# Kernel tuning notes

Measured on AMD Instinct MI355X. Metric: run time of the kernel, lower is better.

Reference implementation:

```python
import jax, jax.numpy as jnp
import numpy as np

B, L, D = 128, 512, 768   # batch, bert tokens, bert hidden
J = 32                    # clause boundaries -> S = J + 1 segments
S = J + 1
DM, DF = 200, 200         # transformer d_model / ffn dim
EPS = 1e-5


def _ln(x, g, b):
    m = x.mean(-1, keepdims=True)
    v = ((x - m) ** 2).mean(-1, keepdims=True)
    return (x - m) / jnp.sqrt(v + EPS) * g + b


def setup_inputs() -> dict:
    key = jax.random.key(0)
    ks = jax.random.split(key, 12)
    sc = 0.02
    hidden_state = jax.random.normal(ks[0], (B, L, D), jnp.float32)
    # strictly increasing, positive clause boundaries < L (non-empty segments)
    seg = L // S  # stride ~= 15 tokens per clause
    jitter = jax.random.randint(ks[1], (B, J), 0, seg).astype(jnp.int32)
    clause_idx = jnp.arange(1, J + 1, dtype=jnp.int32)[None, :] * seg + jitter
    p = lambda k, shp: sc * jax.random.normal(k, shp, jnp.float32)
    z = lambda n: jnp.zeros((n,), jnp.float32)
    return {
        'hidden_state': hidden_state,
        'clause_idx': clause_idx,
        'fc5_w': p(ks[2], (1, D)), 'fc5_b': z(1),
        'fc1_w': p(ks[3], (DM, D)), 'fc1_b': z(DM),
        'attn_in_w': p(ks[4], (3 * DM, DM)), 'attn_in_b': z(3 * DM),
        'attn_out_w': p(ks[5], (DM, DM)), 'attn_out_b': z(DM),
        'ln1_g': jnp.ones((DM,), jnp.float32), 'ln1_b': z(DM),
        'lin1_w': p(ks[6], (DF, DM)), 'lin1_b': z(DF),
        'lin2_w': p(ks[7], (DM, DF)), 'lin2_b': z(DM),
        'ln2_g': jnp.ones((DM,), jnp.float32), 'ln2_b': z(DM),
        'fc_w': p(ks[8], (2, 2 * DM)), 'fc_b': z(2),
    }


def reference(hidden_state, clause_idx, fc5_w, fc5_b, fc1_w, fc1_b,
              attn_in_w, attn_in_b, attn_out_w, attn_out_b,
              ln1_g, ln1_b, lin1_w, lin1_b, lin2_w, lin2_b,
              ln2_g, ln2_b, fc_w, fc_b):
    # ---- ragged per-segment attention pooling (batched_index_select) ----
    t = jnp.arange(L)
    # segment id of each token: number of boundaries <= t  -> [B, L] in [0, S)
    seg_id = jnp.sum(t[None, None, :] >= clause_idx[:, :, None], axis=1)
    scores = jnp.einsum('bld,d->bl', hidden_state, fc5_w[0]) + fc5_b[0]  # fc5
    mask = seg_id[:, None, :] == jnp.arange(S)[None, :, None]            # [B,S,L]
    logits = jnp.where(mask, scores[:, None, :], -jnp.inf)
    w = jax.nn.softmax(logits, axis=-1)        # per-segment softmax over tokens
    pooled = jnp.einsum('bsl,bld->bsd', w, hidden_state)                 # [B,S,D]

    # ---- fc1 + TransformerEncoderLayer (post-norm, 1 head, relu, no dropout)
    x = pooled @ fc1_w.T + fc1_b                                         # [B,S,DM]
    qkv = x @ attn_in_w.T + attn_in_b
    q, k, v = jnp.split(qkv, 3, axis=-1)
    a = jax.nn.softmax(jnp.einsum('bqd,bkd->bqk', q, k) * (1.0 / np.sqrt(DM).item()), axis=-1)
    att = jnp.einsum('bqk,bkd->bqd', a, v) @ attn_out_w.T + attn_out_b
    x = _ln(x + att, ln1_g, ln1_b)
    ff = jax.nn.relu(x @ lin1_w.T + lin1_b) @ lin2_w.T + lin2_b
    x = _ln(x + ff, ln2_g, ln2_b)

    # ---- cat(first-token broadcast, rest) then classifier fc ----
    h = jnp.concatenate([jnp.broadcast_to(x[:, :1, :], (B, S - 1, DM)), x[:, 1:, :]], axis=-1)
    return h @ fc_w.T + fc_b                                             # [B, S-1, 2]
```

## Files before the change

### kernel.cpp

```cpp
#include <hip/hip_runtime.h>

#define NB 128
#define LL 512
#define DD 768
#define JJ 32
#define SS 33
#define DM 200

typedef __attribute__((ext_vector_type(8))) short bf8_t;
typedef __attribute__((ext_vector_type(4))) float f4_t;

#define SB_XF   0
#define SB_QB   61440
#define SB_KB   82944
#define SB_VT   104448
#define SB_Y2   235520
#define SB_BLK  275456

static __device__ __forceinline__ unsigned short f2bf(float f) {
  unsigned u = __float_as_uint(f);
  return (unsigned short)((u + 0x7FFFu + ((u >> 16) & 1u)) >> 16);
}

template<int KS>
static __device__ __forceinline__ f4_t mfma_tile(
    const unsigned short* pa, const unsigned short* pw)
{
  f4_t acc = {0.f, 0.f, 0.f, 0.f};
  bf8_t a = *(const bf8_t*)pa;
  bf8_t w = *(const bf8_t*)pw;
#pragma unroll
  for (int s = 1; s < KS; ++s) {
    bf8_t a2 = *(const bf8_t*)(pa + 32 * s);
    bf8_t w2 = *(const bf8_t*)(pw + 32 * s);
    acc = __builtin_amdgcn_mfma_f32_16x16x32_bf16(a, w, acc, 0, 0, 0);
    a = a2; w = w2;
  }
  acc = __builtin_amdgcn_mfma_f32_16x16x32_bf16(a, w, acc, 0, 0, 0);
  return acc;
}

template<int KS>
static __device__ __forceinline__ f4_t mfma_tile_lds(
    const unsigned short* pa, const unsigned short* pw)
{
  f4_t acc = {0.f, 0.f, 0.f, 0.f};
#pragma unroll
  for (int s = 0; s < KS; ++s) {
    bf8_t a = *(const bf8_t*)(pa + 32 * s);
    bf8_t w = *(const bf8_t*)(pw + 32 * s);
    acc = __builtin_amdgcn_mfma_f32_16x16x32_bf16(a, w, acc, 0, 0, 0);
  }
  return acc;
}

__global__ __launch_bounds__(512) void pc_kernel(
    const float* __restrict__ hidden, const int* __restrict__ clause,
    const float* __restrict__ fc5w, unsigned short* __restrict__ pooled_bf,
    const float* __restrict__ fc1_w, const float* __restrict__ ain_w,
    const float* __restrict__ aout_w, const float* __restrict__ lin1_w,
    const float* __restrict__ lin2_w,
    unsigned short* __restrict__ fc1_wb, unsigned short* __restrict__ ain_wb,
    unsigned short* __restrict__ aout_wb, unsigned short* __restrict__ lin1_wb,
    unsigned short* __restrict__ lin2_wb, char* __restrict__ scratch)
{
  const int tid = threadIdx.x;
  if (blockIdx.x >= NB * SS) {
    int t = (blockIdx.x - NB * SS) * 512 + tid;
    if (t < 208 * 768) {
      int n = t / 768, k = t - n * 768;
      fc1_wb[t] = f2bf((n < 200) ? fc1_w[n * 768 + k] : 0.f);
      return;
    }
    t -= 208 * 768;
    if (t < 608 * 224) {
      int n = t / 224, k = t - n * 224;
      ain_wb[t] = f2bf((n < 600 && k < 200) ? ain_w[n * 200 + k] : 0.f);
      return;
    }
    t -= 608 * 224;
    if (t < 208 * 224) {
      int n = t / 224, k = t - n * 224;
      aout_wb[t] = f2bf((n < 200 && k < 200) ? aout_w[n * 200 + k] : 0.f);
      return;
    }
    t -= 208 * 224;
    if (t < 208 * 224) {
      int n = t / 224, k = t - n * 224;
      lin1_wb[t] = f2bf((n < 200 && k < 200) ? lin1_w[n * 200 + k] : 0.f);
      return;
    }
    t -= 208 * 224;
    if (t < 208 * 224) {
      int n = t / 224, k = t - n * 224;
      lin2_wb[t] = f2bf((n < 200 && k < 200) ? lin2_w[n * 200 + k] : 0.f);
      return;
    }
    t -= 208 * 224;
    if (t < NB * 1344) {
      int b = t / 1344, r = t - b * 1344;
      char* sb = scratch + (size_t)b * SB_BLK;
      const uint4 z = make_uint4(0, 0, 0, 0);
      if (r < 384) {
        int bi = r / 192, rr = r - bi * 192;
        int row = rr >> 2, c = rr & 3;
        int off = (bi == 0) ? SB_QB : SB_KB;
        *(uint4*)((unsigned short*)(sb + off) + row * 224 + 192 + c * 8) = z;
      } else {
        int rr = r - 384;
        int row = rr >> 2, c = rr & 3;
        *(uint4*)((unsigned short*)(sb + SB_VT) + row * 64 + 32 + c * 8) = z;
      }
    }
    return;
  }

  int blk = blockIdx.x;
  int b = blk / SS;
  int s = blk - b * SS;
  int t0 = (s == 0) ? 0 : clause[b * JJ + s - 1];
  int t1 = (s == JJ) ? LL : clause[b * JJ + s];
  int nt = t1 - t0;
  if (nt > 64) nt = 64;
  if (nt < 1) nt = 1;

  __shared__ float wsm[64];
  int wave = tid >> 6, lane = tid & 63;

  const float4* w4 = (const float4*)fc5w;
  for (int t = t0 + wave; t < t0 + nt; t += 8) {
    const float4* hp = (const float4*)(hidden + ((long long)b * LL + t) * DD);
    float acc = 0.f;
#pragma unroll
    for (int i = 0; i < 3; ++i) {
      float4 h = hp[lane + 64 * i];
      float4 w = w4[lane + 64 * i];
      acc += h.x * w.x + h.y * w.y + h.z * w.z + h.w * w.w;
    }
#pragma unroll
    for (int off = 32; off; off >>= 1) acc += __shfl_xor(acc, off);
    if (lane == 0) wsm[t - t0] = acc;
  }
  __syncthreads();

  if (wave == 0) {
    float v = (lane < nt) ? wsm[lane] : -__builtin_inff();
    float mx = v;
#pragma unroll
    for (int off = 32; off; off >>= 1) mx = fmaxf(mx, __shfl_xor(mx, off));
    float e = (lane < nt) ? __expf(v - mx) : 0.f;
    float sm = e;
#pragma unroll
    for (int off = 32; off; off >>= 1) sm += __shfl_xor(sm, off);
    if (lane < nt) wsm[lane] = e / sm;
  }
  __syncthreads();

  if (tid < 384) {
    const float2* base = (const float2*)(hidden + ((long long)b * LL + t0) * DD);
    float2 acc = make_float2(0.f, 0.f);
#pragma unroll 4
    for (int t = 0; t < nt; ++t) {
      float w = wsm[t];
      float2 h = base[t * 384 + tid];
      acc.x = fmaf(w, h.x, acc.x);
      acc.y = fmaf(w, h.y, acc.y);
    }
    ushort2 o;
    o.x = f2bf(acc.x); o.y = f2bf(acc.y);
    *(ushort2*)(pooled_bf + (long long)blk * DD + tid * 2) = o;
  }
}

__global__ __launch_bounds__(512) void k_fc1qkv(
    const unsigned short* __restrict__ pooled,
    const unsigned short* __restrict__ fc1_wb, const float* __restrict__ fc1_b,
    const unsigned short* __restrict__ ain_wb, const float* __restrict__ ain_b,
    char* __restrict__ scratch)
{
  const int b = blockIdx.x / 3, mt = blockIdx.x % 3, m0 = mt * 16;
  const int tid = threadIdx.x, wv = tid >> 6, lane = tid & 63;
  const int col = lane & 15, quad = lane >> 4, koff = quad * 8;

  char* sb = scratch + (size_t)b * SB_BLK;
  float* x_f32 = (float*)(sb + SB_XF);
  unsigned short* q_bf  = (unsigned short*)(sb + SB_QB);
  unsigned short* k_bf  = (unsigned short*)(sb + SB_KB);
  unsigned short* vt_bf = (unsigned short*)(sb + SB_VT);

  __shared__ __align__(16) unsigned short xb[16][232];
  for (int u = tid; u < 16 * 16; u += 512) {
    int row = u >> 4, c = u & 15;
    ((unsigned*)&xb[row][200])[c] = 0u;
  }

  const unsigned short* Ab = pooled + (size_t)b * SS * DD;
  for (int t = wv; t < 13; t += 8) {
    int n0 = t * 16;
    f4_t acc = mfma_tile<24>(Ab + (size_t)(m0 + col) * DD + koff,
                             fc1_wb + (size_t)(n0 + col) * DD + koff);
    int gn = n0 + col;
    if (gn < DM) {
      float bv = fc1_b[gn];
#pragma unroll
      for (int r = 0; r < 4; ++r) {
        int row = quad * 4 + r;
        float v = acc[r] + bv;
        x_f32[(m0 + row) * 208 + gn] = v;
        xb[row][gn] = f2bf(v);
      }
    }
  }
  __syncthreads();

  for (int t = wv; t < 38; t += 8) {
    int n0 = t * 16;
    f4_t acc = mfma_tile_lds<7>(&xb[0][0] + col * 232 + koff,
                                ain_wb + (size_t)(n0 + col) * 224 + koff);
    int gn = n0 + col;
    if (gn < 600) {
      float bv = ain_b[gn];
#pragma unroll
      for (int r = 0; r < 4; ++r) {
        int gm = m0 + quad * 4 + r;
        unsigned short bfv = f2bf(acc[r] + bv);
        if (gn < 200)      q_bf[gm * 224 + gn] = bfv;
        else if (gn < 400) k_bf[gm * 224 + (gn - 200)] = bfv;
        else if (gm < SS)  vt_bf[(gn - 400) * 64 + gm] = bfv;
      }
    }
  }
}

__global__ __launch_bounds__(512) void k_postattn(
    const unsigned short* __restrict__ aout_wb, const float* __restrict__ aout_b,
    const float* __restrict__ ln1_g, const float* __restrict__ ln1_b,
    const unsigned short* __restrict__ lin1_wb, const float* __restrict__ lin1_b,
    const unsigned short* __restrict__ lin2_wb, const float* __restrict__ lin2_b,
    const float* __restrict__ ln2_g, const float* __restrict__ ln2_b,
    char* __restrict__ scratch)
{
  const int b = blockIdx.x / 3, mt = blockIdx.x % 3, m0 = mt * 16;
  const int tid = threadIdx.x, wv = tid >> 6, lane = tid & 63;
  const int col = lane & 15, quad = lane >> 4, koff = quad * 8;

  char* sb = scratch + (size_t)b * SB_BLK;
  const unsigned short* q_bf  = (const unsigned short*)(sb + SB_QB);
  const unsigned short* k_bf  = (const unsigned short*)(sb + SB_KB);
  const unsigned short* vt_bf = (const unsigned short*)(sb + SB_VT);
  const float* x_f32 = (const float*)(sb + SB_XF);
  float* y2g = (float*)(sb + SB_Y2);

  __shared__ float tc[16][211];
  __shared__ __align__(16) unsigned short Pb[16][72];
  __shared__ __align__(16) unsigned short yb[16][232];
  __shared__ __align__(16) unsigned short fb[16][232];
  for (int u = tid; u < 16 * 16; u += 512) {
    int row = u >> 4, c = u & 15;
    ((unsigned*)&yb[row][200])[c] = 0u;
    ((unsigned*)&fb[row][200])[c] = 0u;
  }

  for (int t = wv; t < 3; t += 8) {
    int n0 = t * 16;
    f4_t acc = mfma_tile<7>(q_bf + (m0 + col) * 224 + koff,
                            k_bf + (n0 + col) * 224 + koff);
    int gn = n0 + col;
#pragma unroll
    for (int r = 0; r < 4; ++r)
      tc[quad * 4 + r][gn] = acc[r] * 0.07071067811865475f;
  }
  __syncthreads();

  for (int r = wv; r < 16; r += 8) {
    bool live = (m0 + r) < SS;
    float v = (lane < SS && live) ? tc[r][lane] : -__builtin_inff();
    float mx = v;
#pragma unroll
    for (int off = 32; off; off >>= 1) mx = fmaxf(mx, __shfl_xor(mx, off));
    float e = (lane < SS && live) ? __expf(v - mx) : 0.f;
    float sm = e;
#pragma unroll
    for (int off = 32; off; off >>= 1) sm += __shfl_xor(sm, off);
    Pb[r][lane] = (lane < SS && live) ? f2bf(e / sm) : (unsigned short)0;
  }
  __syncthreads();

  for (int t = wv; t < 13; t += 8) {
    int n0 = t * 16;
    f4_t acc = mfma_tile_lds<2>(&Pb[0][0] + col * 72 + koff,
                                vt_bf + (n0 + col) * 64 + koff);
    int gn = n0 + col;
    if (gn < DM) {
#pragma unroll
      for (int r = 0; r < 4; ++r)
        fb[quad * 4 + r][gn] = f2bf(acc[r]);
    }
  }
  __syncthreads();

  for (int t = wv; t < 13; t += 8) {
    int n0 = t * 16;
    f4_t acc = mfma_tile_lds<7>(&fb[0][0] + col * 232 + koff,
                                aout_wb + (size_t)(n0 + col) * 224 + koff);
    int gn = n0 + col;
    float bv = (gn < DM) ? aout_b[gn] : 0.f;
#pragma unroll
    for (int r = 0; r < 4; ++r) {
      int row = quad * 4 + r;
      float v = acc[r] + bv;
      if (gn < DM) v += x_f32[(m0 + row) * 208 + gn];
      tc[row][gn] = v;
    }
  }
  __syncthreads();

  for (int r = wv; r < 16; r += 8) {
    float* p = &tc[r][0];
    float vals[4]; float s = 0.f;
#pragma unroll
    for (int i = 0; i < 4; ++i) { int k = lane + 64 * i; vals[i] = (k < DM) ? p[k] : 0.f; s += vals[i]; }
#pragma unroll
    for (int off = 32; off; off >>= 1) s += __shfl_xor(s, off);
    float mean = s * (1.f / DM);
    float vs = 0.f;
#pragma unroll
    for (int i = 0; i < 4; ++i) { int k = lane + 64 * i; if (k < DM) { float d = vals[i] - mean; vs += d * d; } }
#pragma unroll
    for (int off = 32; off; off >>= 1) vs += __shfl_xor(vs, off);
    float rstd = rsqrtf(vs * (1.f / DM) + 1e-5f);
#pragma unroll
    for (int i = 0; i < 4; ++i) {
      int k = lane + 64 * i;
      if (k < DM) {
        float o = (vals[i] - mean) * rstd * ln1_g[k] + ln1_b[k];
        p[k] = o;
        yb[r][k] = f2bf(o);
      }
    }
  }
  __syncthreads();

  for (int t = wv; t < 13; t += 8) {
    int n0 = t * 16;
    f4_t acc = mfma_tile_lds<7>(&yb[0][0] + col * 232 + koff,
                                lin1_wb + (size_t)(n0 + col) * 224 + koff);
    int gn = n0 + col;
    if (gn < DM) {
      float bv = lin1_b[gn];
#pragma unroll
      for (int r = 0; r < 4; ++r)
        fb[quad * 4 + r][gn] = f2bf(fmaxf(acc[r] + bv, 0.f));
    }
  }
  __syncthreads();

  for (int t = wv; t < 13; t += 8) {
    int n0 = t * 16;
    f4_t acc = mfma_tile_lds<7>(&fb[0][0] + col * 232 + koff,
                                lin2_wb + (size_t)(n0 + col) * 224 + koff);
    int gn = n0 + col;
    if (gn < DM) {
      float bv = lin2_b[gn];
#pragma unroll
      for (int r = 0; r < 4; ++r) {
        int row = quad * 4 + r;
        tc[row][gn] = acc[r] + bv + tc[row][gn];
      }
    }
  }
  __syncthreads();

  for (int r = wv; r < 16; r += 8) {
    float* p = &tc[r][0];
    float vals[4]; float s = 0.f;
#pragma unroll
    for (int i = 0; i < 4; ++i) { int k = lane + 64 * i; vals[i] = (k < DM) ? p[k] : 0.f; s += vals[i]; }
#pragma unroll
    for (int off = 32; off; off >>= 1) s += __shfl_xor(s, off);
    float mean = s * (1.f / DM);
    float vs = 0.f;
#pragma unroll
    for (int i = 0; i < 4; ++i) { int k = lane + 64 * i; if (k < DM) { float d = vals[i] - mean; vs += d * d; } }
#pragma unroll
    for (int off = 32; off; off >>= 1) vs += __shfl_xor(vs, off);
    float rstd = rsqrtf(vs * (1.f / DM) + 1e-5f);
    int grow = m0 + r;
#pragma unroll
    for (int i = 0; i < 4; ++i) {
      int k = lane + 64 * i;
      if (k < DM) y2g[grow * 208 + k] = (vals[i] - mean) * rstd * ln2_g[k] + ln2_b[k];
    }
  }
}

__global__ __launch_bounds__(256) void k_cls(
    const char* __restrict__ scratch, const float* __restrict__ fcw,
    const float* __restrict__ fcb, float* __restrict__ out)
{
  int gw = blockIdx.x * 4 + (threadIdx.x >> 6);
  int lane = threadIdx.x & 63;
  int b = gw >> 5, j = gw & 31;
  const float* y2 = (const float*)(scratch + (size_t)b * SB_BLK + SB_Y2);
  const float* r0 = y2;
  const float* rj = y2 + (1 + j) * 208;
  float a0 = 0.f, a1 = 0.f;
  for (int k = lane; k < DM; k += 64) {
    float u = r0[k], w = rj[k];
    a0 += u * fcw[k]       + w * fcw[200 + k];
    a1 += u * fcw[400 + k] + w * fcw[600 + k];
  }
#pragma unroll
  for (int off = 32; off; off >>= 1) {
    a0 += __shfl_xor(a0, off);
    a1 += __shfl_xor(a1, off);
  }
  if (lane == 0) {
    out[gw * 2 + 0] = a0 + fcb[0];
    out[gw * 2 + 1] = a1 + fcb[1];
  }
}

extern "C" void kernel_launch(void* const* d_in, const int* in_sizes, int n_in,
                              void* d_out, int out_size, void* d_ws, size_t ws_size,
                              hipStream_t stream)
{
  (void)in_sizes; (void)n_in; (void)out_size; (void)ws_size;
  const float* hidden = (const float*)d_in[0];
  const int*   clause = (const int*)d_in[1];
  const float* fc5_w  = (const float*)d_in[2];
  const float* fc1_w  = (const float*)d_in[4];
  const float* fc1_b  = (const float*)d_in[5];
  const float* ain_w  = (const float*)d_in[6];
  const float* ain_b  = (const float*)d_in[7];
  const float* aout_w = (const float*)d_in[8];
  const float* aout_b = (const float*)d_in[9];
  const float* ln1_g  = (const float*)d_in[10];
  const float* ln1_b  = (const float*)d_in[11];
  const float* lin1_w = (const float*)d_in[12];
  const float* lin1_b = (const float*)d_in[13];
  const float* lin2_w = (const float*)d_in[14];
  const float* lin2_b = (const float*)d_in[15];
  const float* ln2_g  = (const float*)d_in[16];
  const float* ln2_b  = (const float*)d_in[17];
  const float* fc_w   = (const float*)d_in[18];
  const float* fc_b   = (const float*)d_in[19];
  float* out = (float*)d_out;

  char* w8 = (char*)d_ws;
  unsigned short* pooled_bf = (unsigned short*)(w8 + 0);
  char* scratch = w8 + 6520832;
  size_t wbase = 6520832 + (size_t)NB * SB_BLK;
  unsigned short* fc1_wb  = (unsigned short*)(w8 + wbase);
  unsigned short* ain_wb  = (unsigned short*)(w8 + wbase + 319488);
  unsigned short* aout_wb = (unsigned short*)(w8 + wbase + 591872);
  unsigned short* lin1_wb = (unsigned short*)(w8 + wbase + 685056);
  unsigned short* lin2_wb = (unsigned short*)(w8 + wbase + 778240);

  pc_kernel<<<dim3(NB * SS + 1187), 512, 0, stream>>>(
      hidden, clause, fc5_w, pooled_bf,
      fc1_w, ain_w, aout_w, lin1_w, lin2_w,
      fc1_wb, ain_wb, aout_wb, lin1_wb, lin2_wb, scratch);
  k_fc1qkv<<<dim3(NB * 3), 512, 0, stream>>>(pooled_bf, fc1_wb, fc1_b,
      ain_wb, ain_b, scratch);
  k_postattn<<<dim3(NB * 3), 512, 0, stream>>>(aout_wb, aout_b, ln1_g, ln1_b,
      lin1_wb, lin1_b, lin2_wb, lin2_b, ln2_g, ln2_b, scratch);
  k_cls<<<dim3(1024), 256, 0, stream>>>(scratch, fc_w, fc_b, out);
}
```

Baseline: 383.3 us.

## Fuse transformer layers and classifier into one per-batch kernel; stage pooling rows in LDS

Merges the fc1/QKV, attention, FFN and classifier kernels into a single kernel with one block per batch. All intermediates now stay in shared memory instead of global scratch, and three launches are removed. The pooling kernel now reads each token row once, keeps it in LDS in 16-token chunks, and uses an online softmax instead of reading hidden twice. The cost is only 128 blocks for the transformer part, which leaves much of the GPU idle, and about 159KB of LDS per block.

```diff
diff --git a/kernel.cpp b/kernel.cpp
--- a/kernel.cpp
+++ b/kernel.cpp
@@ -9,13 +9,6 @@
 
 typedef __attribute__((ext_vector_type(8))) short bf8_t;
 typedef __attribute__((ext_vector_type(4))) float f4_t;
-
-#define SB_XF   0
-#define SB_QB   61440
-#define SB_KB   82944
-#define SB_VT   104448
-#define SB_Y2   235520
-#define SB_BLK  275456
 
 static __device__ __forceinline__ unsigned short f2bf(float f) {
   unsigned u = __float_as_uint(f);
@@ -53,6 +46,10 @@
   }
   return acc;
 }
+
+#define CVT_FC1 159744
+#define CVT_AIN 136192
+#define CVT_OTH 46592
 
 __global__ __launch_bounds__(512) void pc_kernel(
     const float* __restrict__ hidden, const int* __restrict__ clause,
@@ -62,219 +59,192 @@
     const float* __restrict__ lin2_w,
     unsigned short* __restrict__ fc1_wb, unsigned short* __restrict__ ain_wb,
     unsigned short* __restrict__ aout_wb, unsigned short* __restrict__ lin1_wb,
-    unsigned short* __restrict__ lin2_wb, char* __restrict__ scratch)
+    unsigned short* __restrict__ lin2_wb)
 {
   const int tid = threadIdx.x;
   if (blockIdx.x >= NB * SS) {
     int t = (blockIdx.x - NB * SS) * 512 + tid;
-    if (t < 208 * 768) {
-      int n = t / 768, k = t - n * 768;
-      fc1_wb[t] = f2bf((n < 200) ? fc1_w[n * 768 + k] : 0.f);
-      return;
-    }
-    t -= 208 * 768;
-    if (t < 608 * 224) {
-      int n = t / 224, k = t - n * 224;
-      ain_wb[t] = f2bf((n < 600 && k < 200) ? ain_w[n * 200 + k] : 0.f);
-      return;
-    }
-    t -= 608 * 224;
-    if (t < 208 * 224) {
-      int n = t / 224, k = t - n * 224;
-      aout_wb[t] = f2bf((n < 200 && k < 200) ? aout_w[n * 200 + k] : 0.f);
-      return;
-    }
-    t -= 208 * 224;
-    if (t < 208 * 224) {
-      int n = t / 224, k = t - n * 224;
-      lin1_wb[t] = f2bf((n < 200 && k < 200) ? lin1_w[n * 200 + k] : 0.f);
-      return;
-    }
-    t -= 208 * 224;
-    if (t < 208 * 224) {
-      int n = t / 224, k = t - n * 224;
-      lin2_wb[t] = f2bf((n < 200 && k < 200) ? lin2_w[n * 200 + k] : 0.f);
-      return;
-    }
-    t -= 208 * 224;
-    if (t < NB * 1344) {
-      int b = t / 1344, r = t - b * 1344;
-      char* sb = scratch + (size_t)b * SB_BLK;
-      const uint4 z = make_uint4(0, 0, 0, 0);
-      if (r < 384) {
-        int bi = r / 192, rr = r - bi * 192;
-        int row = rr >> 2, c = rr & 3;
-        int off = (bi == 0) ? SB_QB : SB_KB;
-        *(uint4*)((unsigned short*)(sb + off) + row * 224 + 192 + c * 8) = z;
-      } else {
-        int rr = r - 384;
-        int row = rr >> 2, c = rr & 3;
-        *(uint4*)((unsigned short*)(sb + SB_VT) + row * 64 + 32 + c * 8) = z;
-      }
-    }
+    if (t < CVT_FC1) { int n = t / 768, k = t - n * 768;
+      fc1_wb[t] = f2bf((n < DM) ? fc1_w[n * 768 + k] : 0.f); return; }
+    t -= CVT_FC1;
+    if (t < CVT_AIN) { int n = t / 224, k = t - n * 224;
+      ain_wb[t] = f2bf((n < 600 && k < DM) ? ain_w[n * DM + k] : 0.f); return; }
+    t -= CVT_AIN;
+    if (t < CVT_OTH) { int n = t / 224, k = t - n * 224;
+      aout_wb[t] = f2bf((n < DM && k < DM) ? aout_w[n * DM + k] : 0.f); return; }
+    t -= CVT_OTH;
+    if (t < CVT_OTH) { int n = t / 224, k = t - n * 224;
+      lin1_wb[t] = f2bf((n < DM && k < DM) ? lin1_w[n * DM + k] : 0.f); return; }
+    t -= CVT_OTH;
+    if (t < CVT_OTH) { int n = t / 224, k = t - n * 224;
+      lin2_wb[t] = f2bf((n < DM && k < DM) ? lin2_w[n * DM + k] : 0.f); }
     return;
   }
 
+  __shared__ __align__(16) float rows[16][768];
+  __shared__ float sc[16], wts[16];
+  __shared__ float mprev, denom, rfac;
+
   int blk = blockIdx.x;
-  int b = blk / SS;
-  int s = blk - b * SS;
+  int b = blk / SS, s = blk - b * SS;
   int t0 = (s == 0) ? 0 : clause[b * JJ + s - 1];
   int t1 = (s == JJ) ? LL : clause[b * JJ + s];
   int nt = t1 - t0;
   if (nt > 64) nt = 64;
   if (nt < 1) nt = 1;
 
-  __shared__ float wsm[64];
   int wave = tid >> 6, lane = tid & 63;
-
+  if (tid == 0) { mprev = -__builtin_inff(); denom = 0.f; }
+
+  float2 acc = make_float2(0.f, 0.f);
   const float4* w4 = (const float4*)fc5w;
-  for (int t = t0 + wave; t < t0 + nt; t += 8) {
-    const float4* hp = (const float4*)(hidden + ((long long)b * LL + t) * DD);
-    float acc = 0.f;
-#pragma unroll
-    for (int i = 0; i < 3; ++i) {
-      float4 h = hp[lane + 64 * i];
-      float4 w = w4[lane + 64 * i];
-      acc += h.x * w.x + h.y * w.y + h.z * w.z + h.w * w.w;
-    }
-#pragma unroll
-    for (int off = 32; off; off >>= 1) acc += __shfl_xor(acc, off);
-    if (lane == 0) wsm[t - t0] = acc;
-  }
-  __syncthreads();
-
-  if (wave == 0) {
-    float v = (lane < nt) ? wsm[lane] : -__builtin_inff();
-    float mx = v;
-#pragma unroll
-    for (int off = 32; off; off >>= 1) mx = fmaxf(mx, __shfl_xor(mx, off));
-    float e = (lane < nt) ? __expf(v - mx) : 0.f;
-    float sm = e;
-#pragma unroll
-    for (int off = 32; off; off >>= 1) sm += __shfl_xor(sm, off);
-    if (lane < nt) wsm[lane] = e / sm;
-  }
-  __syncthreads();
-
+  int nchunk = (nt + 15) >> 4;
+  for (int c = 0; c < nchunk; ++c) {
+    int c0 = t0 + (c << 4);
+    int cn = nt - (c << 4); if (cn > 16) cn = 16;
+    for (int tt = wave; tt < cn; tt += 8) {
+      const float4* hp = (const float4*)(hidden + ((long long)b * LL + c0 + tt) * DD);
+      float4 v0 = hp[lane], v1 = hp[lane + 64], v2 = hp[lane + 128];
+      float4 wa = w4[lane], wb = w4[lane + 64], wc = w4[lane + 128];
+      float d = v0.x*wa.x + v0.y*wa.y + v0.z*wa.z + v0.w*wa.w
+              + v1.x*wb.x + v1.y*wb.y + v1.z*wb.z + v1.w*wb.w
+              + v2.x*wc.x + v2.y*wc.y + v2.z*wc.z + v2.w*wc.w;
+#pragma unroll
+      for (int off = 32; off; off >>= 1) d += __shfl_xor(d, off);
+      float4* rp = (float4*)rows[tt];
+      rp[lane] = v0; rp[lane + 64] = v1; rp[lane + 128] = v2;
+      if (lane == 0) sc[tt] = d;
+    }
+    __syncthreads();
+    if (wave == 0) {
+      float v = (lane < cn) ? sc[lane] : -__builtin_inff();
+      float mc = v;
+#pragma unroll
+      for (int off = 32; off; off >>= 1) mc = fmaxf(mc, __shfl_xor(mc, off));
+      float mold = mprev;
+      float mnew = fmaxf(mold, mc);
+      float rr = __expf(mold - mnew);
+      float e = (lane < cn) ? __expf(v - mnew) : 0.f;
+      float sm = e;
+#pragma unroll
+      for (int off = 32; off; off >>= 1) sm += __shfl_xor(sm, off);
+      if (lane < 16) wts[lane] = e;
+      if (lane == 0) { denom = denom * rr + sm; mprev = mnew; rfac = rr; }
+    }
+    __syncthreads();
+    if (tid < 384) {
+      float rr = rfac;
+      acc.x *= rr; acc.y *= rr;
+#pragma unroll 4
+      for (int tt = 0; tt < cn; ++tt) {
+        float w = wts[tt];
+        float2 h = ((const float2*)rows[tt])[tid];
+        acc.x = fmaf(w, h.x, acc.x);
+        acc.y = fmaf(w, h.y, acc.y);
+      }
+    }
+    __syncthreads();
+  }
   if (tid < 384) {
-    const float2* base = (const float2*)(hidden + ((long long)b * LL + t0) * DD);
-    float2 acc = make_float2(0.f, 0.f);
-#pragma unroll 4
-    for (int t = 0; t < nt; ++t) {
-      float w = wsm[t];
-      float2 h = base[t * 384 + tid];
-      acc.x = fmaf(w, h.x, acc.x);
-      acc.y = fmaf(w, h.y, acc.y);
-    }
+    float inv = 1.f / denom;
     ushort2 o;
-    o.x = f2bf(acc.x); o.y = f2bf(acc.y);
-    *(ushort2*)(pooled_bf + (long long)blk * DD + tid * 2) = o;
-  }
-}
-
-__global__ __launch_bounds__(512) void k_fc1qkv(
+    o.x = f2bf(acc.x * inv);
+    o.y = f2bf(acc.y * inv);
+    *(ushort2*)(pooled_bf + (size_t)blk * DD + tid * 2) = o;
+  }
+}
+
+__global__ __launch_bounds__(512) void k_tx(
     const unsigned short* __restrict__ pooled,
     const unsigned short* __restrict__ fc1_wb, const float* __restrict__ fc1_b,
     const unsigned short* __restrict__ ain_wb, const float* __restrict__ ain_b,
-    char* __restrict__ scratch)
-{
-  const int b = blockIdx.x / 3, mt = blockIdx.x % 3, m0 = mt * 16;
-  const int tid = threadIdx.x, wv = tid >> 6, lane = tid & 63;
-  const int col = lane & 15, quad = lane >> 4, koff = quad * 8;
-
-  char* sb = scratch + (size_t)b * SB_BLK;
-  float* x_f32 = (float*)(sb + SB_XF);
-  unsigned short* q_bf  = (unsigned short*)(sb + SB_QB);
-  unsigned short* k_bf  = (unsigned short*)(sb + SB_KB);
-  unsigned short* vt_bf = (unsigned short*)(sb + SB_VT);
-
-  __shared__ __align__(16) unsigned short xb[16][232];
-  for (int u = tid; u < 16 * 16; u += 512) {
-    int row = u >> 4, c = u & 15;
-    ((unsigned*)&xb[row][200])[c] = 0u;
-  }
-
-  const unsigned short* Ab = pooled + (size_t)b * SS * DD;
-  for (int t = wv; t < 13; t += 8) {
-    int n0 = t * 16;
-    f4_t acc = mfma_tile<24>(Ab + (size_t)(m0 + col) * DD + koff,
-                             fc1_wb + (size_t)(n0 + col) * DD + koff);
-    int gn = n0 + col;
-    if (gn < DM) {
-      float bv = fc1_b[gn];
-#pragma unroll
-      for (int r = 0; r < 4; ++r) {
-        int row = quad * 4 + r;
-        float v = acc[r] + bv;
-        x_f32[(m0 + row) * 208 + gn] = v;
-        xb[row][gn] = f2bf(v);
-      }
-    }
-  }
-  __syncthreads();
-
-  for (int t = wv; t < 38; t += 8) {
-    int n0 = t * 16;
-    f4_t acc = mfma_tile_lds<7>(&xb[0][0] + col * 232 + koff,
-                                ain_wb + (size_t)(n0 + col) * 224 + koff);
-    int gn = n0 + col;
-    if (gn < 600) {
-      float bv = ain_b[gn];
-#pragma unroll
-      for (int r = 0; r < 4; ++r) {
-        int gm = m0 + quad * 4 + r;
-        unsigned short bfv = f2bf(acc[r] + bv);
-        if (gn < 200)      q_bf[gm * 224 + gn] = bfv;
-        else if (gn < 400) k_bf[gm * 224 + (gn - 200)] = bfv;
-        else if (gm < SS)  vt_bf[(gn - 400) * 64 + gm] = bfv;
-      }
-    }
-  }
-}
-
-__global__ __launch_bounds__(512) void k_postattn(
     const unsigned short* __restrict__ aout_wb, const float* __restrict__ aout_b,
     const float* __restrict__ ln1_g, const float* __restrict__ ln1_b,
     const unsigned short* __restrict__ lin1_wb, const float* __restrict__ lin1_b,
     const unsigned short* __restrict__ lin2_wb, const float* __restrict__ lin2_b,
     const float* __restrict__ ln2_g, const float* __restrict__ ln2_b,
-    char* __restrict__ scratch)
+    const float* __restrict__ fcw, const float* __restrict__ fcb,
+    float* __restrict__ out)
 {
-  const int b = blockIdx.x / 3, mt = blockIdx.x % 3, m0 = mt * 16;
+  const int b = blockIdx.x;
   const int tid = threadIdx.x, wv = tid >> 6, lane = tid & 63;
   const int col = lane & 15, quad = lane >> 4, koff = quad * 8;
 
-  char* sb = scratch + (size_t)b * SB_BLK;
-  const unsigned short* q_bf  = (const unsigned short*)(sb + SB_QB);
-  const unsigned short* k_bf  = (const unsigned short*)(sb + SB_KB);
-  const unsigned short* vt_bf = (const unsigned short*)(sb + SB_VT);
-  const float* x_f32 = (const float*)(sb + SB_XF);
-  float* y2g = (float*)(sb + SB_Y2);
-
-  __shared__ float tc[16][211];
-  __shared__ __align__(16) unsigned short Pb[16][72];
-  __shared__ __align__(16) unsigned short yb[16][232];
-  __shared__ __align__(16) unsigned short fb[16][232];
-  for (int u = tid; u < 16 * 16; u += 512) {
-    int row = u >> 4, c = u & 15;
-    ((unsigned*)&yb[row][200])[c] = 0u;
-    ((unsigned*)&fb[row][200])[c] = 0u;
-  }
-
-  for (int t = wv; t < 3; t += 8) {
-    int n0 = t * 16;
-    f4_t acc = mfma_tile<7>(q_bf + (m0 + col) * 224 + koff,
-                            k_bf + (n0 + col) * 224 + koff);
-    int gn = n0 + col;
+  __shared__ __align__(16) char smem[159168];
+  float*          xf  = (float*)(smem);
+  unsigned short* xb  = (unsigned short*)(smem + 40128);
+  float*          scb = (float*)(smem + 40128);
+  unsigned short* qb  = (unsigned short*)(smem + 62400);
+  unsigned short* kb  = (unsigned short*)(smem + 84672);
+  unsigned short* Pb  = (unsigned short*)(smem + 62400);
+  unsigned short* yb  = (unsigned short*)(smem + 69312);
+  unsigned short* vt  = (unsigned short*)(smem + 106944);
+  unsigned short* fb  = (unsigned short*)(smem + 136896);
+
+  for (int u = tid; u < 768; u += 512) { int r = u >> 4, c2 = u & 15;
+    ((unsigned*)(xb + r * 232 + 200))[c2] = 0u; }
+  for (int u = tid; u < 768; u += 512) { int r = u >> 4, c2 = u & 15;
+    ((unsigned*)(qb + r * 232 + 200))[c2] = 0u; }
+  for (int u = tid; u < 768; u += 512) { int r = u >> 4, c2 = u & 15;
+    ((unsigned*)(kb + r * 232 + 200))[c2] = 0u; }
+  for (int u = tid; u < 768; u += 512) { int r = u >> 4, c2 = u & 15;
+    ((unsigned*)(fb + r * 232 + 200))[c2] = 0u; }
+  for (int u = tid; u < 7488; u += 512) ((unsigned*)vt)[u] = 0u;
+  __syncthreads();
+
+  const unsigned short* Ab = pooled + (size_t)b * SS * DD;
+  for (int jj = wv; jj < 39; jj += 8) {
+    int mt = jj / 13, t = jj - mt * 13;
+    int m0 = mt * 16, n0 = t * 16, gn = n0 + col;
+    int ar = m0 + col; if (ar > 32) ar = 32;
+    f4_t acc = mfma_tile<24>(Ab + (size_t)ar * DD + koff,
+                             fc1_wb + (size_t)gn * DD + koff);
+    if (gn < DM) {
+      float bv = fc1_b[gn];
+#pragma unroll
+      for (int r = 0; r < 4; ++r) {
+        int row = m0 + quad * 4 + r;
+        float v = acc[r] + bv;
+        xf[row * 209 + gn] = v;
+        xb[row * 232 + gn] = f2bf(v);
+      }
+    }
+  }
+  __syncthreads();
+
+  for (int jj = wv; jj < 114; jj += 8) {
+    int mt = jj / 38, t = jj - mt * 38;
+    int m0 = mt * 16, n0 = t * 16, gn = n0 + col;
+    f4_t acc = mfma_tile_lds<7>(xb + (m0 + col) * 232 + koff,
+                                ain_wb + (size_t)gn * 224 + koff);
+    if (gn < 600) {
+      float bv = ain_b[gn];
+#pragma unroll
+      for (int r = 0; r < 4; ++r) {
+        int gm = m0 + quad * 4 + r;
+        unsigned short bfv = f2bf(acc[r] + bv);
+        if (gn < DM)       qb[gm * 232 + gn] = bfv;
+        else if (gn < 400) kb[gm * 232 + (gn - DM)] = bfv;
+        else if (gm < SS)  vt[(gn - 400) * 72 + gm] = bfv;
+      }
+    }
+  }
+  __syncthreads();
+
+  for (int jj = wv; jj < 9; jj += 8) {
+    int mt = jj / 3, t = jj - mt * 3;
+    int m0 = mt * 16, n0 = t * 16;
+    f4_t acc = mfma_tile_lds<7>(qb + (m0 + col) * 232 + koff,
+                                kb + (n0 + col) * 232 + koff);
 #pragma unroll
     for (int r = 0; r < 4; ++r)
-      tc[quad * 4 + r][gn] = acc[r] * 0.07071067811865475f;
-  }
-  __syncthreads();
-
-  for (int r = wv; r < 16; r += 8) {
-    bool live = (m0 + r) < SS;
-    float v = (lane < SS && live) ? tc[r][lane] : -__builtin_inff();
+      scb[(m0 + quad * 4 + r) * 56 + n0 + col] = acc[r] * 0.07071067811865475f;
+  }
+  __syncthreads();
+
+  for (int r = wv; r < 48; r += 8) {
+    bool live = r < SS;
+    float v = (lane < SS && live) ? scb[r * 56 + lane] : -__builtin_inff();
     float mx = v;
 #pragma unroll
     for (int off = 32; off; off >>= 1) mx = fmaxf(mx, __shfl_xor(mx, off));
@@ -282,50 +252,50 @@
     float sm = e;
 #pragma unroll
     for (int off = 32; off; off >>= 1) sm += __shfl_xor(sm, off);
-    Pb[r][lane] = (lane < SS && live) ? f2bf(e / sm) : (unsigned short)0;
-  }
-  __syncthreads();
-
-  for (int t = wv; t < 13; t += 8) {
-    int n0 = t * 16;
-    f4_t acc = mfma_tile_lds<2>(&Pb[0][0] + col * 72 + koff,
-                                vt_bf + (n0 + col) * 64 + koff);
-    int gn = n0 + col;
+    Pb[r * 72 + lane] = (lane < SS && live) ? f2bf(e / sm) : (unsigned short)0;
+  }
+  __syncthreads();
+
+  for (int jj = wv; jj < 39; jj += 8) {
+    int mt = jj / 13, t = jj - mt * 13;
+    int m0 = mt * 16, n0 = t * 16, gn = n0 + col;
+    f4_t acc = mfma_tile_lds<2>(Pb + (m0 + col) * 72 + koff,
+                                vt + (size_t)gn * 72 + koff);
     if (gn < DM) {
 #pragma unroll
       for (int r = 0; r < 4; ++r)
-        fb[quad * 4 + r][gn] = f2bf(acc[r]);
-    }
-  }
-  __syncthreads();
-
-  for (int t = wv; t < 13; t += 8) {
-    int n0 = t * 16;
-    f4_t acc = mfma_tile_lds<7>(&fb[0][0] + col * 232 + koff,
-                                aout_wb + (size_t)(n0 + col) * 224 + koff);
-    int gn = n0 + col;
-    float bv = (gn < DM) ? aout_b[gn] : 0.f;
-#pragma unroll
-    for (int r = 0; r < 4; ++r) {
-      int row = quad * 4 + r;
-      float v = acc[r] + bv;
-      if (gn < DM) v += x_f32[(m0 + row) * 208 + gn];
-      tc[row][gn] = v;
-    }
-  }
-  __syncthreads();
-
-  for (int r = wv; r < 16; r += 8) {
-    float* p = &tc[r][0];
-    float vals[4]; float s = 0.f;
-#pragma unroll
-    for (int i = 0; i < 4; ++i) { int k = lane + 64 * i; vals[i] = (k < DM) ? p[k] : 0.f; s += vals[i]; }
-#pragma unroll
-    for (int off = 32; off; off >>= 1) s += __shfl_xor(s, off);
-    float mean = s * (1.f / DM);
+        fb[(m0 + quad * 4 + r) * 232 + gn] = f2bf(acc[r]);
+    }
+  }
+  __syncthreads();
+
+  for (int jj = wv; jj < 39; jj += 8) {
+    int mt = jj / 13, t = jj - mt * 13;
+    int m0 = mt * 16, n0 = t * 16, gn = n0 + col;
+    f4_t acc = mfma_tile_lds<7>(fb + (m0 + col) * 232 + koff,
+                                aout_wb + (size_t)gn * 224 + koff);
+    if (gn < DM) {
+      float bv = aout_b[gn];
+#pragma unroll
+      for (int r = 0; r < 4; ++r) {
+        int row = m0 + quad * 4 + r;
+        xf[row * 209 + gn] += acc[r] + bv;
+      }
+    }
+  }
+  __syncthreads();
+
+  for (int r = wv; r < 48; r += 8) {
+    float* p = xf + r * 209;
+    float vals[4]; float sm = 0.f;
+#pragma unroll
+    for (int i = 0; i < 4; ++i) { int k = lane + 64 * i; vals[i] = (k < DM) ? p[k] : 0.f; sm += vals[i]; }
+#pragma unroll
+    for (int off = 32; off; off >>= 1) sm += __shfl_xor(sm, off);
+    float mean = sm * (1.f / DM);
     float vs = 0.f;
 #pragma unroll
-    for (int i = 0; i < 4; ++i) { int k = lane + 64 * i; if (k < DM) { float d = vals[i] - mean; vs += d * d; } }
+    for (int i = 0; i < 4; ++i) { int k = lane + 64 * i; if (k < DM) { float d2 = vals[i] - mean; vs += d2 * d2; } }
 #pragma unroll
     for (int off = 32; off; off >>= 1) vs += __shfl_xor(vs, off);
     float rstd = rsqrtf(vs * (1.f / DM) + 1e-5f);
@@ -335,89 +305,84 @@
       if (k < DM) {
         float o = (vals[i] - mean) * rstd * ln1_g[k] + ln1_b[k];
         p[k] = o;
-        yb[r][k] = f2bf(o);
-      }
-    }
-  }
-  __syncthreads();
-
-  for (int t = wv; t < 13; t += 8) {
-    int n0 = t * 16;
-    f4_t acc = mfma_tile_lds<7>(&yb[0][0] + col * 232 + koff,
-                                lin1_wb + (size_t)(n0 + col) * 224 + koff);
-    int gn = n0 + col;
+        yb[r * 232 + k] = f2bf(o);
+      } else if (k < 232) {
+        yb[r * 232 + k] = 0;
+      }
+    }
+  }
+  __syncthreads();
+
+  for (int jj = wv; jj < 39; jj += 8) {
+    int mt = jj / 13, t = jj - mt * 13;
+    int m0 = mt * 16, n0 = t * 16, gn = n0 + col;
+    f4_t acc = mfma_tile_lds<7>(yb + (m0 + col) * 232 + koff,
+                                lin1_wb + (size_t)gn * 224 + koff);
     if (gn < DM) {
       float bv = lin1_b[gn];
 #pragma unroll
       for (int r = 0; r < 4; ++r)
-        fb[quad * 4 + r][gn] = f2bf(fmaxf(acc[r] + bv, 0.f));
-    }
-  }
-  __syncthreads();
-
-  for (int t = wv; t < 13; t += 8) {
-    int n0 = t * 16;
-    f4_t acc = mfma_tile_lds<7>(&fb[0][0] + col * 232 + koff,
-                                lin2_wb + (size_t)(n0 + col) * 224 + koff);
-    int gn = n0 + col;
+        fb[(m0 + quad * 4 + r) * 232 + gn] = f2bf(fmaxf(acc[r] + bv, 0.f));
+    }
+  }
+  __syncthreads();
+
+  for (int jj = wv; jj < 39; jj += 8) {
+    int mt = jj / 13, t = jj - mt * 13;
+    int m0 = mt * 16, n0 = t * 16, gn = n0 + col;
+    f4_t acc = mfma_tile_lds<7>(fb + (m0 + col) * 232 + koff,
+                                lin2_wb + (size_t)gn * 224 + koff);
     if (gn < DM) {
       float bv = lin2_b[gn];
 #pragma unroll
       for (int r = 0; r < 4; ++r) {
-        int row = quad * 4 + r;
-        tc[row][gn] = acc[r] + bv + tc[row][gn];
-      }
-    }
-  }
-  __syncthreads();
-
-  for (int r = wv; r < 16; r += 8) {
-    float* p = &tc[r][0];
-    float vals[4]; float s = 0.f;
-#pragma unroll
-    for (int i = 0; i < 4; ++i) { int k = lane + 64 * i; vals[i] = (k < DM) ? p[k] : 0.f; s += vals[i]; }
-#pragma unroll
-    for (int off = 32; off; off >>= 1) s += __shfl_xor(s, off);
-    float mean = s * (1.f / DM);
+        int row = m0 + quad * 4 + r;
+        xf[row * 209 + gn] += acc[r] + bv;
+      }
+    }
+  }
+  __syncthreads();
+
+  for (int r = wv; r < 48; r += 8) {
+    float* p = xf + r * 209;
+    float vals[4]; float sm = 0.f;
+#pragma unroll
+    for (int i = 0; i < 4; ++i) { int k = lane + 64 * i; vals[i] = (k < DM) ? p[k] : 0.f; sm += vals[i]; }
+#pragma unroll
+    for (int off = 32; off; off >>= 1) sm += __shfl_xor(sm, off);
+    float mean = sm * (1.f / DM);
     float vs = 0.f;
 #pragma unroll
-    for (int i = 0; i < 4; ++i) { int k = lane + 64 * i; if (k < DM) { float d = vals[i] - mean; vs += d * d; } }
+    for (int i = 0; i < 4; ++i) { int k = lane + 64 * i; if (k < DM) { float d2 = vals[i] - mean; vs += d2 * d2; } }
 #pragma unroll
     for (int off = 32; off; off >>= 1) vs += __shfl_xor(vs, off);
     float rstd = rsqrtf(vs * (1.f / DM) + 1e-5f);
-    int grow = m0 + r;
 #pragma unroll
     for (int i = 0; i < 4; ++i) {
       int k = lane + 64 * i;
-      if (k < DM) y2g[grow * 208 + k] = (vals[i] - mean) * rstd * ln2_g[k] + ln2_b[k];
-    }
-  }
-}
-
-__global__ __launch_bounds__(256) void k_cls(
-    const char* __restrict__ scratch, const float* __restrict__ fcw,
-    const float* __restrict__ fcb, float* __restrict__ out)
-{
-  int gw = blockIdx.x * 4 + (threadIdx.x >> 6);
-  int lane = threadIdx.x & 63;
-  int b = gw >> 5, j = gw & 31;
-  const float* y2 = (const float*)(scratch + (size_t)b * SB_BLK + SB_Y2);
-  const float* r0 = y2;
-  const float* rj = y2 + (1 + j) * 208;
-  float a0 = 0.f, a1 = 0.f;
-  for (int k = lane; k < DM; k += 64) {
-    float u = r0[k], w = rj[k];
-    a0 += u * fcw[k]       + w * fcw[200 + k];
-    a1 += u * fcw[400 + k] + w * fcw[600 + k];
-  }
-#pragma unroll
-  for (int off = 32; off; off >>= 1) {
-    a0 += __shfl_xor(a0, off);
-    a1 += __shfl_xor(a1, off);
-  }
-  if (lane == 0) {
-    out[gw * 2 + 0] = a0 + fcb[0];
-    out[gw * 2 + 1] = a1 + fcb[1];
+      if (k < DM) p[k] = (vals[i] - mean) * rstd * ln2_g[k] + ln2_b[k];
+    }
+  }
+  __syncthreads();
+
+  for (int j = wv; j < 32; j += 8) {
+    const float* r0 = xf;
+    const float* rj = xf + (1 + j) * 209;
+    float a0 = 0.f, a1 = 0.f;
+    for (int k = lane; k < DM; k += 64) {
+      float u = r0[k], w = rj[k];
+      a0 += u * fcw[k]       + w * fcw[200 + k];
+      a1 += u * fcw[400 + k] + w * fcw[600 + k];
+    }
+#pragma unroll
+    for (int off = 32; off; off >>= 1) {
+      a0 += __shfl_xor(a0, off);
+      a1 += __shfl_xor(a1, off);
+    }
+    if (lane == 0) {
+      out[(b * 32 + j) * 2 + 0] = a0 + fcb[0];
+      out[(b * 32 + j) * 2 + 1] = a1 + fcb[1];
+    }
   }
 }
 
@@ -449,21 +414,17 @@
 
   char* w8 = (char*)d_ws;
   unsigned short* pooled_bf = (unsigned short*)(w8 + 0);
-  char* scratch = w8 + 6520832;
-  size_t wbase = 6520832 + (size_t)NB * SB_BLK;
-  unsigned short* fc1_wb  = (unsigned short*)(w8 + wbase);
-  unsigned short* ain_wb  = (unsigned short*)(w8 + wbase + 319488);
-  unsigned short* aout_wb = (unsigned short*)(w8 + wbase + 591872);
-  unsigned short* lin1_wb = (unsigned short*)(w8 + wbase + 685056);
-  unsigned short* lin2_wb = (unsigned short*)(w8 + wbase + 778240);
-
-  pc_kernel<<<dim3(NB * SS + 1187), 512, 0, stream>>>(
+  unsigned short* fc1_wb  = (unsigned short*)(w8 + 6488064);
+  unsigned short* ain_wb  = (unsigned short*)(w8 + 6807552);
+  unsigned short* aout_wb = (unsigned short*)(w8 + 7079936);
+  unsigned short* lin1_wb = (unsigned short*)(w8 + 7173120);
+  unsigned short* lin2_wb = (unsigned short*)(w8 + 7266304);
+
+  pc_kernel<<<dim3(NB * SS + 851), 512, 0, stream>>>(
       hidden, clause, fc5_w, pooled_bf,
       fc1_w, ain_w, aout_w, lin1_w, lin2_w,
-      fc1_wb, ain_wb, aout_wb, lin1_wb, lin2_wb, scratch);
-  k_fc1qkv<<<dim3(NB * 3), 512, 0, stream>>>(pooled_bf, fc1_wb, fc1_b,
-      ain_wb, ain_b, scratch);
-  k_postattn<<<dim3(NB * 3), 512, 0, stream>>>(aout_wb, aout_b, ln1_g, ln1_b,
-      lin1_wb, lin1_b, lin2_wb, lin2_b, ln2_g, ln2_b, scratch);
-  k_cls<<<dim3(1024), 256, 0, stream>>>(scratch, fc_w, fc_b, out);
-}
+      fc1_wb, ain_wb, aout_wb, lin1_wb, lin2_wb);
+  k_tx<<<dim3(NB), 512, 0, stream>>>(pooled_bf, fc1_wb, fc1_b,
+      ain_wb, ain_b, aout_wb, aout_b, ln1_g, ln1_b,
+      lin1_wb, lin1_b, lin2_wb, lin2_b, ln2_g, ln2_b, fc_w, fc_b, out);
+}
```

Result: slower. 407.8 us (+6.4%).
